# Optimization experiments

Measured on AMD Instinct MI355X. Metric: run time of the kernel, lower is better.

Reference implementation:

```python
import jax, jax.numpy as jnp
import numpy as np

TOPK = 2
ROUTE_SCALE = 1.0


def setup_inputs() -> dict:
    key = jax.random.key(0)
    ks = jax.random.split(key, 9)
    B, T, C, E, H = 4, 2048, 1024, 8, 2752
    s = 0.02  # init scale for weights
    return {
        "x": jax.random.normal(ks[0], (B, T, C), dtype=jnp.float32),
        "gate_w": jax.random.normal(ks[1], (E, C), dtype=jnp.float32) * s,
        "expert_bias": jnp.zeros((E,), dtype=jnp.float32),
        "w1": jax.random.normal(ks[2], (E, C, H), dtype=jnp.float32) * s,
        "w2": jax.random.normal(ks[3], (E, H, C), dtype=jnp.float32) * s,
        "w3": jax.random.normal(ks[4], (E, C, H), dtype=jnp.float32) * s,
        "sw1": jax.random.normal(ks[5], (C, H), dtype=jnp.float32) * s,
        "sw2": jax.random.normal(ks[6], (H, C), dtype=jnp.float32) * s,
        "sw3": jax.random.normal(ks[7], (C, H), dtype=jnp.float32) * s,
    }


def reference(x, gate_w, expert_bias, w1, w2, w3, sw1, sw2, sw3):
    B, T, C = x.shape
    E = gate_w.shape[0]
    xf = x.reshape(-1, C)  # (N, C)
    N = xf.shape[0]

    # --- ExpertGate (sigmoid scoring, aux-loss-free, eval mode) ---
    scores = jax.nn.sigmoid(xf @ gate_w.T)            # (N, E), original scores
    routing = scores + expert_bias[None, :]           # bias only affects selection
    _, idx = jax.lax.top_k(routing, TOPK)             # (N, TOPK)
    w = jnp.take_along_axis(scores, idx, axis=1)      # gather original scores
    w = w / (w.sum(axis=-1, keepdims=True) + 1e-8)    # sigmoid normalization
    w = w * ROUTE_SCALE

    # Scatter top-k weights into a dense (N, E) combine matrix
    gates = jnp.zeros((N, E), dtype=xf.dtype)
    gates = gates.at[jnp.arange(N)[:, None], idx].add(w)

    # --- Routed SwiGLU experts (dense compute, gated combine) ---
    y = jnp.zeros_like(xf)
    for e in range(E):  # small fixed loop over experts
        h = jax.nn.silu(xf @ w1[e]) * (xf @ w3[e])    # (N, H)
        y = y + gates[:, e:e + 1] * (h @ w2[e])

    # --- Shared expert (always on) ---
    y = y + (jax.nn.silu(xf @ sw1) * (xf @ sw3)) @ sw2

    return y.reshape(B, T, C)
```

## Files before the change

kernel.cpp:

```cpp
#include <hip/hip_runtime.h>
#include <hip/hip_bf16.h>
#include <stdint.h>

#define E_ 8
#define C_ 1024
#define H_ 2752
#define NTOK 8192
#define CAP_ROWS 18432
#define ROUTED_MB 72
#define SHARED_MB 32
#define SHARED_HBASE 18432
#define HROWS 26624

typedef unsigned short u16;
typedef __attribute__((ext_vector_type(8))) short bf16x8;
typedef __attribute__((ext_vector_type(4))) float f32x4;

static constexpr size_t SZ_XB    = (size_t)NTOK * C_ * 2;
static constexpr size_t SZ_WT    = (size_t)E_ * H_ * C_ * 2;
static constexpr size_t SZ_SWT   = (size_t)H_ * C_ * 2;
static constexpr size_t SZ_H     = (size_t)HROWS * H_ * 2;

static constexpr size_t OFF_XB   = 0;
static constexpr size_t OFF_W1T  = OFF_XB   + SZ_XB;
static constexpr size_t OFF_W3T  = OFF_W1T  + SZ_WT;
static constexpr size_t OFF_W2T  = OFF_W3T  + SZ_WT;
static constexpr size_t OFF_SW1T = OFF_W2T  + SZ_WT;
static constexpr size_t OFF_SW3T = OFF_SW1T + SZ_SWT;
static constexpr size_t OFF_SW2T = OFF_SW3T + SZ_SWT;
static constexpr size_t OFF_H    = OFF_SW2T + SZ_SWT;
static constexpr size_t OFF_ZP   = OFF_H    + SZ_H;
static constexpr size_t OFF_RIDX = OFF_ZP   + 16384;
static constexpr size_t OFF_RW   = OFF_RIDX + (size_t)NTOK*2*4;
static constexpr size_t OFF_OFFS = OFF_RW   + (size_t)NTOK*2*4;
static constexpr size_t OFF_PTOK = OFF_OFFS + 64;
static constexpr size_t OFF_PW   = OFF_PTOK + (size_t)CAP_ROWS*4;
static constexpr size_t WS_NEED  = OFF_PW   + (size_t)CAP_ROWS*4;

__device__ __forceinline__ u16 f2bf(float f) {
  union { float f; uint32_t u; } v; v.f = f;
  uint32_t r = v.u + 0x7FFFu + ((v.u >> 16) & 1u);
  return (u16)(r >> 16);
}

__device__ __forceinline__ void gld16(const void* g, void* l) {
  uint32_t lo = (uint32_t)(uintptr_t)l;
  lo = __builtin_amdgcn_readfirstlane(lo);
  __builtin_amdgcn_global_load_lds(
      (const __attribute__((address_space(1))) void*)g,
      (__attribute__((address_space(3))) void*)(uintptr_t)lo, 16, 0, 0);
}

#define MFMA16(A,B,C) __builtin_amdgcn_mfma_f32_16x16x32_bf16((A),(B),(C),0,0,0)
#define BARX() do { asm volatile("" ::: "memory"); __builtin_amdgcn_s_barrier(); \
                    asm volatile("" ::: "memory"); } while (0)
#define VMC(N) asm volatile("s_waitcnt vmcnt(" #N ")" ::: "memory")

__global__ __launch_bounds__(256) void gate_kernel(
    const float* __restrict__ x, const float* __restrict__ gw,
    const float* __restrict__ bias, u16* __restrict__ xb,
    int* __restrict__ ridx, float* __restrict__ rw)
{
  const int n = blockIdx.x, t = threadIdx.x;
  const float4 v = *(const float4*)(x + (size_t)n * C_ + t * 4);
  union { u16 u[4]; uint2 d; } pk;
  pk.u[0] = f2bf(v.x); pk.u[1] = f2bf(v.y); pk.u[2] = f2bf(v.z); pk.u[3] = f2bf(v.w);
  *(uint2*)(xb + (size_t)n * C_ + t * 4) = pk.d;

  float p[E_];
#pragma unroll
  for (int e = 0; e < E_; ++e) {
    const float4 g = *(const float4*)(gw + (size_t)e * C_ + t * 4);
    p[e] = v.x * g.x + v.y * g.y + v.z * g.z + v.w * g.w;
  }
#pragma unroll
  for (int e = 0; e < E_; ++e)
    for (int off = 32; off > 0; off >>= 1) p[e] += __shfl_down(p[e], off);

  __shared__ float red[4][E_];
  const int wv = t >> 6;
  if ((t & 63) == 0) {
#pragma unroll
    for (int e = 0; e < E_; ++e) red[wv][e] = p[e];
  }
  __syncthreads();
  if (t == 0) {
    float sc[E_], rt[E_];
#pragma unroll
    for (int e = 0; e < E_; ++e) {
      const float d = red[0][e] + red[1][e] + red[2][e] + red[3][e];
      const float s = 1.f / (1.f + expf(-d));
      sc[e] = s; rt[e] = s + bias[e];
    }
    int i0 = 0; float b0 = rt[0];
#pragma unroll
    for (int e = 1; e < E_; ++e) if (rt[e] > b0) { b0 = rt[e]; i0 = e; }
    int i1 = -1; float b1 = -1e30f;
#pragma unroll
    for (int e = 0; e < E_; ++e) if (e != i0 && rt[e] > b1) { b1 = rt[e]; i1 = e; }
    const float s0 = sc[i0], s1 = sc[i1];
    const float inv = 1.f / (s0 + s1 + 1e-8f);
    ridx[2 * n] = i0; ridx[2 * n + 1] = i1;
    rw[2 * n] = s0 * inv; rw[2 * n + 1] = s1 * inv;
  }
}

__global__ __launch_bounds__(256) void transpose_cs_kernel(
    const float* __restrict__ w1, const float* __restrict__ w3,
    const float* __restrict__ sw1, const float* __restrict__ sw3,
    u16* __restrict__ w1t, u16* __restrict__ w3t,
    u16* __restrict__ sw1t, u16* __restrict__ sw3t)
{
  const int z = blockIdx.z;
  const float* src; u16* dst;
  if      (z < 8)  { src = w1 + (size_t)z * C_ * H_;       dst = w1t + (size_t)z * H_ * C_; }
  else if (z < 16) { src = w3 + (size_t)(z - 8) * C_ * H_; dst = w3t + (size_t)(z - 8) * H_ * C_; }
  else if (z == 16){ src = sw1; dst = sw1t; }
  else             { src = sw3; dst = sw3t; }
  __shared__ float tile[32][33];
  const int tx = threadIdx.x, ty = threadIdx.y;
  const int s0 = blockIdx.x * 32;
  const int r0 = blockIdx.y * 32;
#pragma unroll
  for (int i = 0; i < 4; ++i)
    tile[ty + 8 * i][tx] = src[(size_t)(r0 + ty + 8 * i) * H_ + s0 + tx];
  __syncthreads();
#pragma unroll
  for (int i = 0; i < 4; ++i)
    dst[(size_t)(s0 + ty + 8 * i) * C_ + r0 + tx] = f2bf(tile[tx][ty + 8 * i]);
}

__global__ __launch_bounds__(256) void transpose_sc_kernel(
    const float* __restrict__ w2, const float* __restrict__ sw2,
    u16* __restrict__ w2t, u16* __restrict__ sw2t)
{
  const int z = blockIdx.z;
  const float* src; u16* dst;
  if (z < 8) { src = w2 + (size_t)z * H_ * C_; dst = w2t + (size_t)z * C_ * H_; }
  else       { src = sw2; dst = sw2t; }
  __shared__ float tile[32][33];
  const int tx = threadIdx.x, ty = threadIdx.y;
  const int s0 = blockIdx.x * 32;
  const int r0 = blockIdx.y * 32;
#pragma unroll
  for (int i = 0; i < 4; ++i)
    tile[ty + 8 * i][tx] = src[(size_t)(r0 + ty + 8 * i) * C_ + s0 + tx];
  __syncthreads();
#pragma unroll
  for (int i = 0; i < 4; ++i)
    dst[(size_t)(s0 + ty + 8 * i) * H_ + r0 + tx] = f2bf(tile[tx][ty + 8 * i]);
}

__global__ __launch_bounds__(256) void route_scan_kernel(
    const int* __restrict__ ridx, const float* __restrict__ rw,
    int* __restrict__ offsets, int* __restrict__ perm_tok, float* __restrict__ perm_w)
{
  __shared__ int cnt[256][E_];
  __shared__ int pref[E_][257];
  __shared__ int offs[E_ + 1];
  __shared__ int totals[E_];
  const int t = threadIdx.x;
#pragma unroll
  for (int e = 0; e < E_; ++e) cnt[t][e] = 0;
  for (int j = 0; j < 64; ++j) { const int e = ridx[t * 64 + j]; cnt[t][e]++; }
  __syncthreads();
  if (t < E_) {
    int run = 0;
    for (int i = 0; i < 256; ++i) { pref[t][i] = run; run += cnt[i][t]; }
    totals[t] = run; pref[t][256] = run;
  }
  __syncthreads();
  if (t == 0) {
    int o = 0;
    for (int e = 0; e < E_; ++e) { offs[e] = o; o += (totals[e] + 255) & ~255; }
    offs[E_] = o;
    for (int i = 0; i <= E_; ++i) offsets[i] = offs[i];
  }
  __syncthreads();
#pragma unroll
  for (int e = 0; e < E_; ++e) cnt[t][e] = offs[e] + pref[e][t];
  for (int j = 0; j < 64; ++j) {
    const int a = t * 64 + j;
    const int e = ridx[a];
    const int p = cnt[t][e]++;
    perm_tok[p] = a >> 1;
    perm_w[p] = rw[a];
  }
  __syncthreads();
  for (int e = 0; e < E_; ++e) {
    for (int p = offs[e] + totals[e] + t; p < offs[e + 1]; p += 256) {
      perm_tok[p] = 0; perm_w[p] = 0.f;
    }
  }
}

__global__ __launch_bounds__(512, 2) void gemm1_8p(
    const u16* __restrict__ xb, const u16* __restrict__ w1t_all,
    const u16* __restrict__ w3t_all, const u16* __restrict__ sw1t,
    const u16* __restrict__ sw3t, u16* __restrict__ hbuf,
    const int* __restrict__ offsets, const int* __restrict__ ptok)
{
  __shared__ char lds[131072];
  const int t = threadIdx.x;
  const int bx = blockIdx.x;
  const int n0 = blockIdx.y * 128;

  const u16 *b1w, *b3w; int row0; size_t hr0; int gather;
  if (bx < ROUTED_MB) {
    row0 = bx * 256;
    if (row0 >= offsets[8]) return;
    int e = 0;
#pragma unroll
    for (int i = 0; i < 7; ++i) if (row0 >= offsets[i + 1]) e = i + 1;
    b1w = w1t_all + (size_t)e * (H_ * C_);
    b3w = w3t_all + (size_t)e * (H_ * C_);
    hr0 = (size_t)row0; gather = 1;
  } else {
    row0 = (bx - ROUTED_MB) * 256;
    b1w = sw1t; b3w = sw3t; hr0 = (size_t)SHARED_HBASE + row0; gather = 0;
  }

  const int sr = t >> 2;
  const int sc = (((t & 3) ^ ((t >> 3) & 3)) << 4);
  const int ta0 = gather ? ptok[row0 + sr]       : (row0 + sr);
  const int ta1 = gather ? ptok[row0 + 128 + sr] : (row0 + 128 + sr);
  const char* aS0 = (const char*)xb + (size_t)ta0 * 2048 + sc;
  const char* aS1 = (const char*)xb + (size_t)ta1 * 2048 + sc;
  int nb = n0 + sr; if (nb > H_ - 1) nb = H_ - 1;
  const char* b1S = (const char*)b1w + (size_t)nb * 2048 + sc;
  const char* b3S = (const char*)b3w + (size_t)nb * 2048 + sc;
  const int wb = (t >> 6) << 10;
  char* ldsp = (char*)lds;

#define ARG(kt,kh)  ((((kt)&1)*2+(kh))*16384)
#define B1RG(kt,kh) (65536 + ((((kt)&1)*2+(kh))*8192))
#define B3RG(kt,kh) (98304 + ((((kt)&1)*2+(kh))*8192))
#define SA(kt,kh) do { const int go=(kt)*128+(kh)*64; \
  gld16(aS0+go, ldsp+ARG(kt,kh)+wb); gld16(aS1+go, ldsp+ARG(kt,kh)+8192+wb); } while(0)
#define SB(kt,kh) do { const int go=(kt)*128+(kh)*64; \
  gld16(b1S+go, ldsp+B1RG(kt,kh)+wb); gld16(b3S+go, ldsp+B3RG(kt,kh)+wb); } while(0)

  const int lane = t & 63, l15 = lane & 15, lhi = lane >> 4;
  const int wv = t >> 6, wm = wv >> 2, wn = wv & 3;
  const int cswz = ((lhi ^ ((l15 >> 1) & 3)) << 4);
  int aoff[8], boff[2];
#pragma unroll
  for (int mf = 0; mf < 8; ++mf) aoff[mf] = (wm * 128 + mf * 16 + l15) * 64 + cswz;
#pragma unroll
  for (int nf = 0; nf < 2; ++nf) boff[nf] = (wn * 32 + nf * 16 + l15) * 64 + cswz;

  bf16x8 a[4], rb1[2], rb3[2];
  f32x4 acc1[8][2], acc3[8][2];
#pragma unroll
  for (int i = 0; i < 8; ++i)
#pragma unroll
    for (int j = 0; j < 2; ++j) { acc1[i][j] = f32x4{0,0,0,0}; acc3[i][j] = f32x4{0,0,0,0}; }

#define LB(kt,kh) do { \
  rb1[0]=*(const bf16x8*)(ldsp+B1RG(kt,kh)+boff[0]); \
  rb1[1]=*(const bf16x8*)(ldsp+B1RG(kt,kh)+boff[1]); \
  rb3[0]=*(const bf16x8*)(ldsp+B3RG(kt,kh)+boff[0]); \
  rb3[1]=*(const bf16x8*)(ldsp+B3RG(kt,kh)+boff[1]); } while(0)
#define LA(kt,kh,mh) do { \
  a[0]=*(const bf16x8*)(ldsp+ARG(kt,kh)+aoff[(mh)*4+0]); \
  a[1]=*(const bf16x8*)(ldsp+ARG(kt,kh)+aoff[(mh)*4+1]); \
  a[2]=*(const bf16x8*)(ldsp+ARG(kt,kh)+aoff[(mh)*4+2]); \
  a[3]=*(const bf16x8*)(ldsp+ARG(kt,kh)+aoff[(mh)*4+3]); } while(0)
#define MM(mh) do { __builtin_amdgcn_s_setprio(1); \
  _Pragma("unroll") for (int mf = 0; mf < 4; ++mf) \
    _Pragma("unroll") for (int nf = 0; nf < 2; ++nf) { \
      acc1[(mh)*4+mf][nf] = MFMA16(a[mf], rb1[nf], acc1[(mh)*4+mf][nf]); \
      acc3[(mh)*4+mf][nf] = MFMA16(a[mf], rb3[nf], acc3[(mh)*4+mf][nf]); } \
  __builtin_amdgcn_s_setprio(0); } while(0)

  SA(0,0); SA(0,1); SB(0,0); SB(0,1); SA(1,0); SB(1,0);
  VMC(4); BARX();

#pragma unroll 1
  for (int i = 0; i < 8; ++i) {
    const int k0 = 2*i, k1 = k0+1, k2 = k0+2, k3 = k0+3;
    const bool more = (i < 7);
    LB(k0,0); LA(k0,0,0); SA(k1,1); SB(k1,1);
    BARX(); MM(0); BARX();
    LA(k0,0,1);
    BARX(); MM(1); BARX();
    LB(k0,1); LA(k0,1,0); if (more) SA(k2,0);
    BARX(); MM(0); BARX();
    LA(k0,1,1); if (more) SB(k2,0);
    BARX(); MM(1);
    if (more) { VMC(4); } else { VMC(0); }
    BARX();
    LB(k1,0); LA(k1,0,0); if (more) { SA(k2,1); SB(k2,1); }
    BARX(); MM(0); BARX();
    LA(k1,0,1);
    BARX(); MM(1); BARX();
    LB(k1,1); LA(k1,1,0); if (more) SA(k3,0);
    BARX(); MM(0); BARX();
    LA(k1,1,1); if (more) SB(k3,0);
    BARX(); MM(1);
    if (more) { VMC(4); }
    BARX();
  }

  const int rb_ = wm * 128 + lhi * 4;
  const int cb_ = n0 + wn * 32 + l15;
#pragma unroll
  for (int mf = 0; mf < 8; ++mf)
#pragma unroll
    for (int q = 0; q < 4; ++q) {
      const int r = rb_ + mf * 16 + q;
      u16* hrow = hbuf + (hr0 + r) * H_;
#pragma unroll
      for (int nf = 0; nf < 2; ++nf) {
        const int c = cb_ + nf * 16;
        if (c < H_) {
          const float v1 = acc1[mf][nf][q], v3 = acc3[mf][nf][q];
          hrow[c] = f2bf((v1 / (1.f + __expf(-v1))) * v3);
        }
      }
    }
#undef ARG
#undef B1RG
#undef B3RG
#undef SA
#undef SB
#undef LB
#undef LA
#undef MM
}

template<int MODE>
__global__ __launch_bounds__(512, 2) void gemm2_8p(
    const u16* __restrict__ hbuf, const u16* __restrict__ w2t_all,
    float* __restrict__ y, const int* __restrict__ offsets,
    const int* __restrict__ ptok, const float* __restrict__ pw,
    const char* __restrict__ zp)
{
  __shared__ char lds[98304];
  const int t = threadIdx.x;
  const int bx = blockIdx.x;
  const int n0 = blockIdx.y * 128;

  int row0 = bx * 256; size_t hr0; const u16* bW;
  if (MODE == 1) {
    if (row0 >= offsets[8]) return;
    int e = 0;
#pragma unroll
    for (int i = 0; i < 7; ++i) if (row0 >= offsets[i + 1]) e = i + 1;
    bW = w2t_all + (size_t)e * (C_ * H_);
    hr0 = (size_t)row0;
  } else {
    bW = w2t_all;
    hr0 = (size_t)SHARED_HBASE + row0;
  }

  const int sr = t >> 2;
  const int sc = (((t & 3) ^ ((t >> 3) & 3)) << 4);
  const char* aS0 = (const char*)hbuf + (hr0 + sr) * (size_t)(H_ * 2) + sc;
  const char* aS1 = (const char*)hbuf + (hr0 + 128 + sr) * (size_t)(H_ * 2) + sc;
  const char* bS  = (const char*)bW + (size_t)(n0 + sr) * (H_ * 2) + sc;
  const int wb = (t >> 6) << 10;
  char* ldsp = (char*)lds;
  const char* zpa = zp + t * 16;

#define A2RG(kt,kh) ((((kt)&1)*2+(kh))*16384)
#define B2RG(kt,kh) (65536 + ((((kt)&1)*2+(kh))*8192))
#define SA2(kt,kh) do { if ((kt) < 43) { const int go=(kt)*128+(kh)*64; \
    gld16(aS0+go, ldsp+A2RG(kt,kh)+wb); gld16(aS1+go, ldsp+A2RG(kt,kh)+8192+wb); } \
  else { gld16(zpa, ldsp+A2RG(kt,kh)+wb); gld16(zpa, ldsp+A2RG(kt,kh)+8192+wb); } } while(0)
#define SB2(kt,kh) do { if ((kt) < 43) { const int go=(kt)*128+(kh)*64; \
    gld16(bS+go, ldsp+B2RG(kt,kh)+wb); } \
  else { gld16(zpa, ldsp+B2RG(kt,kh)+wb); } } while(0)

  const int lane = t & 63, l15 = lane & 15, lhi = lane >> 4;
  const int wv = t >> 6, wm = wv >> 2, wn = wv & 3;
  const int cswz = ((lhi ^ ((l15 >> 1) & 3)) << 4);
  int aoff[8], boff[2];
#pragma unroll
  for (int mf = 0; mf < 8; ++mf) aoff[mf] = (wm * 128 + mf * 16 + l15) * 64 + cswz;
#pragma unroll
  for (int nf = 0; nf < 2; ++nf) boff[nf] = (wn * 32 + nf * 16 + l15) * 64 + cswz;

  bf16x8 a8[8], rb[2];
  f32x4 acc[8][2];
#pragma unroll
  for (int i = 0; i < 8; ++i)
#pragma unroll
    for (int j = 0; j < 2; ++j) acc[i][j] = f32x4{0,0,0,0};

#define LB2(kt,kh) do { \
  rb[0]=*(const bf16x8*)(ldsp+B2RG(kt,kh)+boff[0]); \
  rb[1]=*(const bf16x8*)(ldsp+B2RG(kt,kh)+boff[1]); } while(0)
#define LA8(kt,kh) do { \
  _Pragma("unroll") for (int mf = 0; mf < 8; ++mf) \
    a8[mf]=*(const bf16x8*)(ldsp+A2RG(kt,kh)+aoff[mf]); } while(0)
#define MM2() do { __builtin_amdgcn_s_setprio(1); \
  _Pragma("unroll") for (int mf = 0; mf < 8; ++mf) \
    _Pragma("unroll") for (int nf = 0; nf < 2; ++nf) \
      acc[mf][nf] = MFMA16(a8[mf], rb[nf], acc[mf][nf]); \
  __builtin_amdgcn_s_setprio(0); } while(0)

  SA2(0,0); SA2(0,1); SB2(0,0); SB2(0,1); SA2(1,0); SB2(1,0);
  VMC(3); BARX();

#pragma unroll 1
  for (int i = 0; i < 22; ++i) {
    const int k0 = 2*i, k1 = k0+1, k2 = k0+2, k3 = k0+3;
    const bool more = (i < 21);
    LB2(k0,0); LA8(k0,0); SA2(k1,1); SB2(k1,1);
    BARX(); MM2(); BARX();
    LB2(k0,1); LA8(k0,1); if (more) { SA2(k2,0); SB2(k2,0); }
    BARX(); MM2();
    if (more) { VMC(3); } else { VMC(0); }
    BARX();
    LB2(k1,0); LA8(k1,0); if (more) { SA2(k2,1); SB2(k2,1); }
    BARX(); MM2(); BARX();
    LB2(k1,1); LA8(k1,1); if (more) { SA2(k3,0); SB2(k3,0); }
    BARX(); MM2();
    if (more) { VMC(3); }
    BARX();
  }

  const int rb_ = wm * 128 + lhi * 4;
  const int cb_ = n0 + wn * 32 + l15;
#pragma unroll
  for (int mf = 0; mf < 8; ++mf)
#pragma unroll
    for (int q = 0; q < 4; ++q) {
      const int r = rb_ + mf * 16 + q;
      if (MODE == 0) {
        float* yr = y + (size_t)(row0 + r) * C_;
#pragma unroll
        for (int nf = 0; nf < 2; ++nf) yr[cb_ + nf * 16] = acc[mf][nf][q];
      } else {
        const float wgt = pw[row0 + r];
        if (wgt != 0.f) {
          const int tok = ptok[row0 + r];
          float* yr = y + (size_t)tok * C_;
#pragma unroll
          for (int nf = 0; nf < 2; ++nf)
            atomicAdd(yr + cb_ + nf * 16, wgt * acc[mf][nf][q]);
        }
      }
    }
#undef A2RG
#undef B2RG
#undef SA2
#undef SB2
#undef LB2
#undef LA8
#undef MM2
}

extern "C" void kernel_launch(void* const* d_in, const int* in_sizes, int n_in,
                              void* d_out, int out_size, void* d_ws, size_t ws_size,
                              hipStream_t stream)
{
  const float* x    = (const float*)d_in[0];
  const float* gw   = (const float*)d_in[1];
  const float* bias = (const float*)d_in[2];
  const float* w1   = (const float*)d_in[3];
  const float* w2   = (const float*)d_in[4];
  const float* w3   = (const float*)d_in[5];
  const float* sw1  = (const float*)d_in[6];
  const float* sw2  = (const float*)d_in[7];
  const float* sw3  = (const float*)d_in[8];
  float* y = (float*)d_out;
  char* ws = (char*)d_ws;
  if (ws_size < WS_NEED) return;

  u16*   xb    = (u16*)(ws + OFF_XB);
  u16*   w1t   = (u16*)(ws + OFF_W1T);
  u16*   w3t   = (u16*)(ws + OFF_W3T);
  u16*   w2t   = (u16*)(ws + OFF_W2T);
  u16*   sw1t  = (u16*)(ws + OFF_SW1T);
  u16*   sw3t  = (u16*)(ws + OFF_SW3T);
  u16*   sw2t  = (u16*)(ws + OFF_SW2T);
  u16*   hbuf  = (u16*)(ws + OFF_H);
  char*  zp    = ws + OFF_ZP;
  int*   ridx  = (int*)(ws + OFF_RIDX);
  float* rwt   = (float*)(ws + OFF_RW);
  int*   offs  = (int*)(ws + OFF_OFFS);
  int*   ptok  = (int*)(ws + OFF_PTOK);
  float* pw    = (float*)(ws + OFF_PW);

  hipMemsetAsync(zp, 0, 16384, stream);
  gate_kernel<<<NTOK, 256, 0, stream>>>(x, gw, bias, xb, ridx, rwt);
  transpose_cs_kernel<<<dim3(H_ / 32, C_ / 32, 18), dim3(32, 8), 0, stream>>>(
      w1, w3, sw1, sw3, w1t, w3t, sw1t, sw3t);
  transpose_sc_kernel<<<dim3(C_ / 32, H_ / 32, 9), dim3(32, 8), 0, stream>>>(
      w2, sw2, w2t, sw2t);
  route_scan_kernel<<<1, 256, 0, stream>>>(ridx, rwt, offs, ptok, pw);

  gemm1_8p<<<dim3(ROUTED_MB + SHARED_MB, 22), 512, 0, stream>>>(
      xb, w1t, w3t, sw1t, sw3t, hbuf, offs, ptok);
  gemm2_8p<0><<<dim3(SHARED_MB, 8), 512, 0, stream>>>(
      hbuf, sw2t, y, offs, ptok, pw, zp);
  gemm2_8p<1><<<dim3(ROUTED_MB, 8), 512, 0, stream>>>(
      hbuf, w2t, y, offs, ptok, pw, zp);
}
```

Measured before the change: 757.4 us.

## Restructure GEMM K-loop into two-phase pipeline with full 64-wide K tiles

```diff
diff --git a/kernel.cpp b/kernel.cpp
--- a/kernel.cpp
+++ b/kernel.cpp
@@ -194,7 +194,7 @@
   }
 }
 
-__global__ __launch_bounds__(512, 2) void gemm1_8p(
+__global__ __launch_bounds__(512, 2) void gemm1_2p(
     const u16* __restrict__ xb, const u16* __restrict__ w1t_all,
     const u16* __restrict__ w3t_all, const u16* __restrict__ sw1t,
     const u16* __restrict__ sw3t, u16* __restrict__ hbuf,
@@ -220,85 +220,74 @@
     b1w = sw1t; b3w = sw3t; hr0 = (size_t)SHARED_HBASE + row0; gather = 0;
   }
 
-  const int sr = t >> 2;
-  const int sc = (((t & 3) ^ ((t >> 3) & 3)) << 4);
-  const int ta0 = gather ? ptok[row0 + sr]       : (row0 + sr);
-  const int ta1 = gather ? ptok[row0 + 128 + sr] : (row0 + 128 + sr);
-  const char* aS0 = (const char*)xb + (size_t)ta0 * 2048 + sc;
-  const char* aS1 = (const char*)xb + (size_t)ta1 * 2048 + sc;
-  int nb = n0 + sr; if (nb > H_ - 1) nb = H_ - 1;
-  const char* b1S = (const char*)b1w + (size_t)nb * 2048 + sc;
-  const char* b3S = (const char*)b3w + (size_t)nb * 2048 + sc;
+  const int sr = t >> 3;
+  const int scb = (((t & 7) ^ (sr & 7)) << 4);
+  const char* aS[4]; const char* b1S[2]; const char* b3S[2];
+#pragma unroll
+  for (int c = 0; c < 4; ++c) {
+    const int r = row0 + c * 64 + sr;
+    const int tok = gather ? ptok[r] : r;
+    aS[c] = (const char*)xb + (size_t)tok * 2048 + scb;
+  }
+#pragma unroll
+  for (int c = 0; c < 2; ++c) {
+    int nb = n0 + c * 64 + sr; if (nb > H_ - 1) nb = H_ - 1;
+    b1S[c] = (const char*)b1w + (size_t)nb * 2048 + scb;
+    b3S[c] = (const char*)b3w + (size_t)nb * 2048 + scb;
+  }
   const int wb = (t >> 6) << 10;
   char* ldsp = (char*)lds;
 
-#define ARG(kt,kh)  ((((kt)&1)*2+(kh))*16384)
-#define B1RG(kt,kh) (65536 + ((((kt)&1)*2+(kh))*8192))
-#define B3RG(kt,kh) (98304 + ((((kt)&1)*2+(kh))*8192))
-#define SA(kt,kh) do { const int go=(kt)*128+(kh)*64; \
-  gld16(aS0+go, ldsp+ARG(kt,kh)+wb); gld16(aS1+go, ldsp+ARG(kt,kh)+8192+wb); } while(0)
-#define SB(kt,kh) do { const int go=(kt)*128+(kh)*64; \
-  gld16(b1S+go, ldsp+B1RG(kt,kh)+wb); gld16(b3S+go, ldsp+B3RG(kt,kh)+wb); } while(0)
+#define SA1(kt,c) gld16(aS[c]  + (kt)*128, ldsp + ((kt)&1)*32768 + (c)*8192 + wb)
+#define SB1(kt,c) gld16(b1S[c] + (kt)*128, ldsp + 65536 + ((kt)&1)*16384 + (c)*8192 + wb)
+#define SB3(kt,c) gld16(b3S[c] + (kt)*128, ldsp + 98304 + ((kt)&1)*16384 + (c)*8192 + wb)
 
   const int lane = t & 63, l15 = lane & 15, lhi = lane >> 4;
   const int wv = t >> 6, wm = wv >> 2, wn = wv & 3;
-  const int cswz = ((lhi ^ ((l15 >> 1) & 3)) << 4);
-  int aoff[8], boff[2];
-#pragma unroll
-  for (int mf = 0; mf < 8; ++mf) aoff[mf] = (wm * 128 + mf * 16 + l15) * 64 + cswz;
-#pragma unroll
-  for (int nf = 0; nf < 2; ++nf) boff[nf] = (wn * 32 + nf * 16 + l15) * 64 + cswz;
-
-  bf16x8 a[4], rb1[2], rb3[2];
+  const int co0 = ((lhi ^ (l15 & 7)) << 4);
+  const int co1 = (((4 + lhi) ^ (l15 & 7)) << 4);
+  const int arow = wm * 16384 + l15 * 128;
+  const int brow = wn * 4096 + l15 * 128;
+
+  bf16x8 a[4][2], rb1[2][2], rb3[2][2];
   f32x4 acc1[8][2], acc3[8][2];
 #pragma unroll
   for (int i = 0; i < 8; ++i)
 #pragma unroll
     for (int j = 0; j < 2; ++j) { acc1[i][j] = f32x4{0,0,0,0}; acc3[i][j] = f32x4{0,0,0,0}; }
 
-#define LB(kt,kh) do { \
-  rb1[0]=*(const bf16x8*)(ldsp+B1RG(kt,kh)+boff[0]); \
-  rb1[1]=*(const bf16x8*)(ldsp+B1RG(kt,kh)+boff[1]); \
-  rb3[0]=*(const bf16x8*)(ldsp+B3RG(kt,kh)+boff[0]); \
-  rb3[1]=*(const bf16x8*)(ldsp+B3RG(kt,kh)+boff[1]); } while(0)
-#define LA(kt,kh,mh) do { \
-  a[0]=*(const bf16x8*)(ldsp+ARG(kt,kh)+aoff[(mh)*4+0]); \
-  a[1]=*(const bf16x8*)(ldsp+ARG(kt,kh)+aoff[(mh)*4+1]); \
-  a[2]=*(const bf16x8*)(ldsp+ARG(kt,kh)+aoff[(mh)*4+2]); \
-  a[3]=*(const bf16x8*)(ldsp+ARG(kt,kh)+aoff[(mh)*4+3]); } while(0)
+#define LB(p) do { _Pragma("unroll") for (int nf = 0; nf < 2; ++nf) { \
+  rb1[nf][0] = *(const bf16x8*)(ldsp + 65536 + (p)*16384 + brow + nf*2048 + co0); \
+  rb1[nf][1] = *(const bf16x8*)(ldsp + 65536 + (p)*16384 + brow + nf*2048 + co1); \
+  rb3[nf][0] = *(const bf16x8*)(ldsp + 98304 + (p)*16384 + brow + nf*2048 + co0); \
+  rb3[nf][1] = *(const bf16x8*)(ldsp + 98304 + (p)*16384 + brow + nf*2048 + co1); } } while (0)
+#define LA(p,mh) do { _Pragma("unroll") for (int mf = 0; mf < 4; ++mf) { \
+  a[mf][0] = *(const bf16x8*)(ldsp + (p)*32768 + arow + ((mh)*4+mf)*2048 + co0); \
+  a[mf][1] = *(const bf16x8*)(ldsp + (p)*32768 + arow + ((mh)*4+mf)*2048 + co1); } } while (0)
 #define MM(mh) do { __builtin_amdgcn_s_setprio(1); \
-  _Pragma("unroll") for (int mf = 0; mf < 4; ++mf) \
-    _Pragma("unroll") for (int nf = 0; nf < 2; ++nf) { \
-      acc1[(mh)*4+mf][nf] = MFMA16(a[mf], rb1[nf], acc1[(mh)*4+mf][nf]); \
-      acc3[(mh)*4+mf][nf] = MFMA16(a[mf], rb3[nf], acc3[(mh)*4+mf][nf]); } \
-  __builtin_amdgcn_s_setprio(0); } while(0)
-
-  SA(0,0); SA(0,1); SB(0,0); SB(0,1); SA(1,0); SB(1,0);
-  VMC(4); BARX();
+  _Pragma("unroll") for (int kh = 0; kh < 2; ++kh) \
+    _Pragma("unroll") for (int mf = 0; mf < 4; ++mf) \
+      _Pragma("unroll") for (int nf = 0; nf < 2; ++nf) { \
+        acc1[(mh)*4+mf][nf] = MFMA16(a[mf][kh], rb1[nf][kh], acc1[(mh)*4+mf][nf]); \
+        acc3[(mh)*4+mf][nf] = MFMA16(a[mf][kh], rb3[nf][kh], acc3[(mh)*4+mf][nf]); } \
+  __builtin_amdgcn_s_setprio(0); } while (0)
+
+  SA1(0,0); SA1(0,2); SB1(0,0); SB1(0,1); SB3(0,0); SB3(0,1); SA1(0,1); SA1(0,3);
+  VMC(2); BARX();
 
 #pragma unroll 1
-  for (int i = 0; i < 8; ++i) {
-    const int k0 = 2*i, k1 = k0+1, k2 = k0+2, k3 = k0+3;
-    const bool more = (i < 7);
-    LB(k0,0); LA(k0,0,0); SA(k1,1); SB(k1,1);
-    BARX(); MM(0); BARX();
-    LA(k0,0,1);
-    BARX(); MM(1); BARX();
-    LB(k0,1); LA(k0,1,0); if (more) SA(k2,0);
-    BARX(); MM(0); BARX();
-    LA(k0,1,1); if (more) SB(k2,0);
-    BARX(); MM(1);
+  for (int j = 0; j < 16; ++j) {
+    const int p = j & 1;
+    const bool more = (j < 15);
+    LB(p); LA(p, 0);
+    if (more) { SA1(j+1,0); SA1(j+1,2); SB1(j+1,0); SB1(j+1,1); }
+    BARX(); MM(0);
     if (more) { VMC(4); } else { VMC(0); }
     BARX();
-    LB(k1,0); LA(k1,0,0); if (more) { SA(k2,1); SB(k2,1); }
-    BARX(); MM(0); BARX();
-    LA(k1,0,1);
-    BARX(); MM(1); BARX();
-    LB(k1,1); LA(k1,1,0); if (more) SA(k3,0);
-    BARX(); MM(0); BARX();
-    LA(k1,1,1); if (more) SB(k3,0);
+    LA(p, 1);
+    if (more) { SB3(j+1,0); SB3(j+1,1); SA1(j+1,1); SA1(j+1,3); }
     BARX(); MM(1);
-    if (more) { VMC(4); }
+    if (more) { VMC(2); }
     BARX();
   }
 
@@ -319,18 +308,16 @@
         }
       }
     }
-#undef ARG
-#undef B1RG
-#undef B3RG
-#undef SA
-#undef SB
+#undef SA1
+#undef SB1
+#undef SB3
 #undef LB
 #undef LA
 #undef MM
 }
 
 template<int MODE>
-__global__ __launch_bounds__(512, 2) void gemm2_8p(
+__global__ __launch_bounds__(512, 2) void gemm2_2p(
     const u16* __restrict__ hbuf, const u16* __restrict__ w2t_all,
     float* __restrict__ y, const int* __restrict__ offsets,
     const int* __restrict__ ptok, const float* __restrict__ pw,
@@ -354,70 +341,67 @@
     hr0 = (size_t)SHARED_HBASE + row0;
   }
 
-  const int sr = t >> 2;
-  const int sc = (((t & 3) ^ ((t >> 3) & 3)) << 4);
-  const char* aS0 = (const char*)hbuf + (hr0 + sr) * (size_t)(H_ * 2) + sc;
-  const char* aS1 = (const char*)hbuf + (hr0 + 128 + sr) * (size_t)(H_ * 2) + sc;
-  const char* bS  = (const char*)bW + (size_t)(n0 + sr) * (H_ * 2) + sc;
+  const int sr = t >> 3;
+  const int scb = (((t & 7) ^ (sr & 7)) << 4);
+  const char* aS[4]; const char* bS[2];
+#pragma unroll
+  for (int c = 0; c < 4; ++c)
+    aS[c] = (const char*)hbuf + (hr0 + c * 64 + sr) * (size_t)(H_ * 2) + scb;
+#pragma unroll
+  for (int c = 0; c < 2; ++c)
+    bS[c] = (const char*)bW + (size_t)(n0 + c * 64 + sr) * (H_ * 2) + scb;
   const int wb = (t >> 6) << 10;
   char* ldsp = (char*)lds;
   const char* zpa = zp + t * 16;
 
-#define A2RG(kt,kh) ((((kt)&1)*2+(kh))*16384)
-#define B2RG(kt,kh) (65536 + ((((kt)&1)*2+(kh))*8192))
-#define SA2(kt,kh) do { if ((kt) < 43) { const int go=(kt)*128+(kh)*64; \
-    gld16(aS0+go, ldsp+A2RG(kt,kh)+wb); gld16(aS1+go, ldsp+A2RG(kt,kh)+8192+wb); } \
-  else { gld16(zpa, ldsp+A2RG(kt,kh)+wb); gld16(zpa, ldsp+A2RG(kt,kh)+8192+wb); } } while(0)
-#define SB2(kt,kh) do { if ((kt) < 43) { const int go=(kt)*128+(kh)*64; \
-    gld16(bS+go, ldsp+B2RG(kt,kh)+wb); } \
-  else { gld16(zpa, ldsp+B2RG(kt,kh)+wb); } } while(0)
+#define SA2(kt,c) do { const char* s_ = ((kt) < 43) ? (aS[c] + (kt)*128) : zpa; \
+  gld16(s_, ldsp + ((kt)&1)*32768 + (c)*8192 + wb); } while (0)
+#define SB2(kt,c) do { const char* s_ = ((kt) < 43) ? (bS[c] + (kt)*128) : zpa; \
+  gld16(s_, ldsp + 65536 + ((kt)&1)*16384 + (c)*8192 + wb); } while (0)
 
   const int lane = t & 63, l15 = lane & 15, lhi = lane >> 4;
   const int wv = t >> 6, wm = wv >> 2, wn = wv & 3;
-  const int cswz = ((lhi ^ ((l15 >> 1) & 3)) << 4);
-  int aoff[8], boff[2];
-#pragma unroll
-  for (int mf = 0; mf < 8; ++mf) aoff[mf] = (wm * 128 + mf * 16 + l15) * 64 + cswz;
-#pragma unroll
-  for (int nf = 0; nf < 2; ++nf) boff[nf] = (wn * 32 + nf * 16 + l15) * 64 + cswz;
-
-  bf16x8 a8[8], rb[2];
+  const int co0 = ((lhi ^ (l15 & 7)) << 4);
+  const int co1 = (((4 + lhi) ^ (l15 & 7)) << 4);
+  const int arow = wm * 16384 + l15 * 128;
+  const int brow = wn * 4096 + l15 * 128;
+
+  bf16x8 a[4][2], rb[2][2];
   f32x4 acc[8][2];
 #pragma unroll
   for (int i = 0; i < 8; ++i)
 #pragma unroll
     for (int j = 0; j < 2; ++j) acc[i][j] = f32x4{0,0,0,0};
 
-#define LB2(kt,kh) do { \
-  rb[0]=*(const bf16x8*)(ldsp+B2RG(kt,kh)+boff[0]); \
-  rb[1]=*(const bf16x8*)(ldsp+B2RG(kt,kh)+boff[1]); } while(0)
-#define LA8(kt,kh) do { \
-  _Pragma("unroll") for (int mf = 0; mf < 8; ++mf) \
-    a8[mf]=*(const bf16x8*)(ldsp+A2RG(kt,kh)+aoff[mf]); } while(0)
-#define MM2() do { __builtin_amdgcn_s_setprio(1); \
-  _Pragma("unroll") for (int mf = 0; mf < 8; ++mf) \
-    _Pragma("unroll") for (int nf = 0; nf < 2; ++nf) \
-      acc[mf][nf] = MFMA16(a8[mf], rb[nf], acc[mf][nf]); \
-  __builtin_amdgcn_s_setprio(0); } while(0)
-
-  SA2(0,0); SA2(0,1); SB2(0,0); SB2(0,1); SA2(1,0); SB2(1,0);
-  VMC(3); BARX();
+#define LB2(p) do { _Pragma("unroll") for (int nf = 0; nf < 2; ++nf) { \
+  rb[nf][0] = *(const bf16x8*)(ldsp + 65536 + (p)*16384 + brow + nf*2048 + co0); \
+  rb[nf][1] = *(const bf16x8*)(ldsp + 65536 + (p)*16384 + brow + nf*2048 + co1); } } while (0)
+#define LA2(p,mh) do { _Pragma("unroll") for (int mf = 0; mf < 4; ++mf) { \
+  a[mf][0] = *(const bf16x8*)(ldsp + (p)*32768 + arow + ((mh)*4+mf)*2048 + co0); \
+  a[mf][1] = *(const bf16x8*)(ldsp + (p)*32768 + arow + ((mh)*4+mf)*2048 + co1); } } while (0)
+#define MM2(mh) do { __builtin_amdgcn_s_setprio(1); \
+  _Pragma("unroll") for (int kh = 0; kh < 2; ++kh) \
+    _Pragma("unroll") for (int mf = 0; mf < 4; ++mf) \
+      _Pragma("unroll") for (int nf = 0; nf < 2; ++nf) \
+        acc[(mh)*4+mf][nf] = MFMA16(a[mf][kh], rb[nf][kh], acc[(mh)*4+mf][nf]); \
+  __builtin_amdgcn_s_setprio(0); } while (0)
+
+  SA2(0,0); SA2(0,2); SB2(0,0); SB2(0,1); SA2(0,1); SA2(0,3);
+  VMC(2); BARX();
 
 #pragma unroll 1
-  for (int i = 0; i < 22; ++i) {
-    const int k0 = 2*i, k1 = k0+1, k2 = k0+2, k3 = k0+3;
-    const bool more = (i < 21);
-    LB2(k0,0); LA8(k0,0); SA2(k1,1); SB2(k1,1);
-    BARX(); MM2(); BARX();
-    LB2(k0,1); LA8(k0,1); if (more) { SA2(k2,0); SB2(k2,0); }
-    BARX(); MM2();
+  for (int j = 0; j < 44; ++j) {
+    const int p = j & 1;
+    const bool more = (j < 43);
+    LB2(p); LA2(p, 0);
+    if (more) { SA2(j+1,0); SA2(j+1,2); SB2(j+1,0); }
+    BARX(); MM2(0);
     if (more) { VMC(3); } else { VMC(0); }
     BARX();
-    LB2(k1,0); LA8(k1,0); if (more) { SA2(k2,1); SB2(k2,1); }
-    BARX(); MM2(); BARX();
-    LB2(k1,1); LA8(k1,1); if (more) { SA2(k3,0); SB2(k3,0); }
-    BARX(); MM2();
-    if (more) { VMC(3); }
+    LA2(p, 1);
+    if (more) { SB2(j+1,1); SA2(j+1,1); SA2(j+1,3); }
+    BARX(); MM2(1);
+    if (more) { VMC(2); }
     BARX();
   }
 
@@ -443,12 +427,10 @@
         }
       }
     }
-#undef A2RG
-#undef B2RG
 #undef SA2
 #undef SB2
 #undef LB2
-#undef LA8
+#undef LA2
 #undef MM2
 }
 
@@ -492,10 +474,10 @@
       w2, sw2, w2t, sw2t);
   route_scan_kernel<<<1, 256, 0, stream>>>(ridx, rwt, offs, ptok, pw);
 
-  gemm1_8p<<<dim3(ROUTED_MB + SHARED_MB, 22), 512, 0, stream>>>(
+  gemm1_2p<<<dim3(ROUTED_MB + SHARED_MB, 22), 512, 0, stream>>>(
       xb, w1t, w3t, sw1t, sw3t, hbuf, offs, ptok);
-  gemm2_8p<0><<<dim3(SHARED_MB, 8), 512, 0, stream>>>(
+  gemm2_2p<0><<<dim3(SHARED_MB, 8), 512, 0, stream>>>(
       hbuf, sw2t, y, offs, ptok, pw, zp);
-  gemm2_8p<1><<<dim3(ROUTED_MB, 8), 512, 0, stream>>>(
+  gemm2_2p<1><<<dim3(ROUTED_MB, 8), 512, 0, stream>>>(
       hbuf, w2t, y, offs, ptok, pw, zp);
 }
```

New measurement: 789.3 us. 4.2% more time.
